# Optimization experiments

Measured on AMD Instinct MI355X. Metric: run time of the kernel, lower is better.

The kernel has to match this reference:

```python
import jax, jax.numpy as jnp
import numpy as np

NUM_HEADS = 12
NUM_PATCHES = 4096
DIM = 768
IN_DIMS = DIM // NUM_HEADS
SCALE = NUM_PATCHES ** (-0.5)
LN_EPS = 1e-5


def setup_inputs() -> dict:
    key = jax.random.key(0)
    ks = jax.random.split(key, 14)
    s = 0.02
    return {
        "x": jax.random.normal(ks[0], (16, NUM_PATCHES, DIM), dtype=jnp.float32),
        "wq": jax.random.normal(ks[1], (DIM, DIM), dtype=jnp.float32) * s,
        "bq": jnp.zeros((DIM,), dtype=jnp.float32),
        "wk": jax.random.normal(ks[2], (DIM, DIM), dtype=jnp.float32) * s,
        "bk": jnp.zeros((DIM,), dtype=jnp.float32),
        "w_g": jax.random.normal(ks[3], (NUM_PATCHES,), dtype=jnp.float32),
        "w_fc": jax.random.normal(ks[4], (IN_DIMS, DIM), dtype=jnp.float32) * s,
        "b_fc": jnp.zeros((DIM,), dtype=jnp.float32),
        "w_fc2": jax.random.normal(ks[5], (NUM_HEADS, NUM_HEADS), dtype=jnp.float32) * s,
        "b_fc2": jnp.zeros((NUM_HEADS,), dtype=jnp.float32),
        "w_proj": jax.random.normal(ks[6], (DIM, DIM), dtype=jnp.float32) * s,
        "b_proj": jnp.zeros((DIM,), dtype=jnp.float32),
        "gamma": jnp.ones((DIM,), dtype=jnp.float32),
        "beta": jnp.zeros((DIM,), dtype=jnp.float32),
    }


def layernorm(x, gamma, beta):
    mu = jnp.mean(x, axis=-1, keepdims=True)
    var = jnp.mean(jnp.square(x - mu), axis=-1, keepdims=True)
    return (x - mu) * jax.lax.rsqrt(var + LN_EPS) * gamma + beta


def reference(x, wq, bq, wk, bk, w_g, w_fc, b_fc, w_fc2, b_fc2, w_proj, b_proj, gamma, beta):
    bs, n, d = x.shape
    q = x @ wq + bq                      # (b,n,d)  fc_q
    k = x @ wk + bk                      # (b,n,d)  fc_k (reassigned x in torch)
    # query_weight = (q^T @ w_g)^T -> (b,1,d); softmax over channel dim
    qw = jnp.einsum("bnd,n->bd", q, w_g) * SCALE
    A = jax.nn.softmax(qw, axis=-1)      # (b,d)
    # G = sum_n(A * k): A is constant over n, so equals A * sum_n k
    G = A * jnp.sum(k, axis=1)           # (b,d)
    # sigmoid gating chain on pooled q
    dv = jnp.mean(q, axis=1)             # (b,d)   AdaptiveAvgPool over n
    dv = dv.reshape(bs, NUM_HEADS, IN_DIMS)
    dv = jax.nn.gelu(dv @ w_fc + b_fc, approximate=False)   # (b,H,d)
    dv = dv.reshape(bs, d, NUM_HEADS)    # reshape (not transpose), as in torch
    dv = dv @ w_fc2 + b_fc2              # (b,d,H)
    dv = jax.nn.sigmoid(jnp.mean(dv, axis=-1))               # (b,d)
    G = G * dv                           # (b,d)
    out = (G[:, None, :] * k) @ w_proj + b_proj + layernorm(k, gamma, beta)
    return out
```

## Files before the change

### kernel.cpp

```cpp
#include <hip/hip_runtime.h>
#include <hip/hip_bf16.h>
#include <math.h>

#define NB 16
#define NP 4096
#define DDIM 768
#define MTOT (NB*NP)
#define N1 1536
#define BM 128
#define BN 128
#define BK 64
#define SCALEF 0.015625f
#define LNEPS 1e-5f

typedef __attribute__((ext_vector_type(8))) short bf16x8;
typedef __attribute__((ext_vector_type(4))) float f32x4;
typedef __attribute__((ext_vector_type(4))) unsigned int u32x4;
typedef unsigned short us;

__device__ __forceinline__ us f2b(float f){
  union { float f; unsigned int u; } v; v.f = f;
  unsigned int u = v.u;
  unsigned int r = (u + 0x7FFFu + ((u >> 16) & 1u)) >> 16;
  return (us)r;
}
__device__ __forceinline__ unsigned int pack2(float a, float b){
  return (unsigned int)f2b(a) | ((unsigned int)f2b(b) << 16);
}
__device__ __forceinline__ float b2f(us h){
  union { unsigned int u; float f; } v; v.u = ((unsigned int)h) << 16;
  return v.f;
}
__device__ __forceinline__ float b2f_lo(unsigned int u){
  union { unsigned int x; float f; } v; v.x = u << 16; return v.f;
}
__device__ __forceinline__ float b2f_hi(unsigned int u){
  union { unsigned int x; float f; } v; v.x = u & 0xFFFF0000u; return v.f;
}

typedef __attribute__((address_space(1))) const unsigned int gas_u32;
typedef __attribute__((address_space(3))) unsigned int las_u32;
__device__ __forceinline__ void gl2lds16(const void* g, void* l){
  __builtin_amdgcn_global_load_lds((gas_u32*)g, (las_u32*)l, 16, 0, 0);
}

__global__ __launch_bounds__(256) void convert_x(const float* __restrict__ x,
                                                 us* __restrict__ xb){
  size_t i = ((size_t)blockIdx.x * 256 + threadIdx.x) * 8;
  const float4* s = reinterpret_cast<const float4*>(x + i);
  float4 a = s[0], b = s[1];
  u32x4 w;
  w[0] = pack2(a.x, a.y); w[1] = pack2(a.z, a.w);
  w[2] = pack2(b.x, b.y); w[3] = pack2(b.z, b.w);
  *reinterpret_cast<u32x4*>(xb + i) = w;
}

__global__ __launch_bounds__(256) void prep_w(const float* __restrict__ wq,
                                              const float* __restrict__ wk,
                                              const float* __restrict__ wp,
                                              us* __restrict__ wt1,
                                              us* __restrict__ wt2){
  int idx = blockIdx.x * 256 + threadIdx.x;
  const int tot1 = N1 * DDIM;
  if (idx < tot1){
    int n = idx / DDIM, k = idx % DDIM;
    float v = (n < DDIM) ? wq[k * DDIM + n] : wk[k * DDIM + (n - DDIM)];
    wt1[idx] = f2b(v);
  }
  int idx2 = idx - tot1;
  if (idx2 >= 0 && idx2 < DDIM * DDIM){
    int n = idx2 / DDIM, k = idx2 % DDIM;
    wt2[idx2] = f2b(wp[k * DDIM + n]);
  }
}

__global__ __launch_bounds__(256) void prep_wb(const us* __restrict__ wt2,
                                               const float* __restrict__ g,
                                               us* __restrict__ wbuf){
  size_t idx = (size_t)blockIdx.x * 256 + threadIdx.x;
  int d = (int)(idx % DDIM);
  size_t nd = idx / DDIM;
  int n = (int)(nd % DDIM);
  int b = (int)(nd / DDIM);
  float v = b2f(wt2[n * DDIM + d]) * g[(size_t)b * DDIM + d];
  wbuf[idx] = f2b(v);
}

__global__ __launch_bounds__(256) void ln_stats(const us* __restrict__ kin,
                                                float2* __restrict__ rstats){
  int row = blockIdx.x * 4 + (threadIdx.x >> 6);
  int l = threadIdx.x & 63;
  const us* rp = kin + (size_t)row * DDIM;
  float s = 0.f, q = 0.f;
  bf16x8 v = *reinterpret_cast<const bf16x8*>(rp + l * 8);
  #pragma unroll
  for (int j = 0; j < 8; ++j){ float f = b2f((us)v[j]); s += f; q += f * f; }
  uint2 w2 = *reinterpret_cast<const uint2*>(rp + 512 + l * 4);
  { float f0 = b2f_lo(w2.x), f1 = b2f_hi(w2.x), f2 = b2f_lo(w2.y), f3 = b2f_hi(w2.y);
    s += f0 + f1 + f2 + f3; q += f0*f0 + f1*f1 + f2*f2 + f3*f3; }
  #pragma unroll
  for (int off = 1; off < 64; off <<= 1){
    s += __shfl_xor(s, off);
    q += __shfl_xor(q, off);
  }
  if (l == 0){
    float mu = s * (1.0f / DDIM);
    float var = q * (1.0f / DDIM) - mu * mu;
    rstats[row] = make_float2(mu, rsqrtf(var + LNEPS));
  }
}

__global__ __launch_bounds__(256) void gemm_qk(
    const us* __restrict__ xb, const us* __restrict__ wt1,
    const float* __restrict__ bq, const float* __restrict__ bk,
    const float* __restrict__ w_g,
    us* __restrict__ kout,
    float* __restrict__ qwp, float* __restrict__ qsp, float* __restrict__ ksp)
{
  __shared__ us lds[2][2][BM * BK];

  int bid = blockIdx.x;
  int swz = (bid & 7) * ((int)gridDim.x >> 3) + (bid >> 3);
  const int NBN = N1 / BN;
  int bn = swz % NBN, bm = swz / NBN;
  int m0 = bm * BM, n0 = bn * BN;
  int t = threadIdx.x, lane = t & 63, wave = t >> 6;
  int wm = wave >> 1, wn = wave & 1;
  int lr = lane & 15, lh = lane >> 4;

  const us* pa[4]; const us* pb[4];
  #pragma unroll
  for (int i = 0; i < 4; ++i){
    int c = wave * 4 + i;
    int u = c * 64 + lane;
    int row = u >> 3, cell = u & 7;
    pa[i] = xb  + (size_t)(m0 + row) * DDIM + cell * 8;
    pb[i] = wt1 + (size_t)(n0 + row) * DDIM + cell * 8;
  }
  auto stage = [&](int bufi, int ks){
    int ko = ks * BK;
    #pragma unroll
    for (int i = 0; i < 4; ++i){
      int c = wave * 4 + i;
      gl2lds16(pa[i] + ko, &lds[bufi][0][c * 512]);
      gl2lds16(pb[i] + ko, &lds[bufi][1][c * 512]);
    }
  };

  f32x4 acc[4][4] = {};
  stage(0, 0);
  __syncthreads();
  int buf = 0;
  for (int ks = 0; ks < DDIM / BK; ++ks){
    if (ks < DDIM / BK - 1) stage(buf ^ 1, ks + 1);
    #pragma unroll
    for (int kk = 0; kk < 2; ++kk){
      bf16x8 af[4], bfr[4];
      #pragma unroll
      for (int i = 0; i < 4; ++i)
        af[i] = *reinterpret_cast<const bf16x8*>(&lds[buf][0][(wm*64 + i*16 + lr)*BK + kk*32 + lh*8]);
      #pragma unroll
      for (int i = 0; i < 4; ++i)
        bfr[i] = *reinterpret_cast<const bf16x8*>(&lds[buf][1][(wn*64 + i*16 + lr)*BK + kk*32 + lh*8]);
      #pragma unroll
      for (int i = 0; i < 4; ++i)
        #pragma unroll
        for (int j = 0; j < 4; ++j)
          acc[i][j] = __builtin_amdgcn_mfma_f32_16x16x32_bf16(af[i], bfr[j], acc[i][j], 0, 0, 0);
    }
    __syncthreads();
    buf ^= 1;
  }

  bool is_q = (n0 < DDIM);
  int b = m0 / NP, mc = (m0 % NP) / BM;
  float* part0 = reinterpret_cast<float*>(&lds[1][0][0]);
  float* part1 = part0 + BM * 8;
  us* stash = &lds[0][0][0];

  float wgv[4][4];
  if (is_q){
    #pragma unroll
    for (int mf = 0; mf < 4; ++mf)
      #pragma unroll
      for (int r = 0; r < 4; ++r)
        wgv[mf][r] = w_g[(m0 & (NP - 1)) + wm*64 + mf*16 + lh*4 + r];
  }

  float r0a[4], r1a[4];
  #pragma unroll
  for (int nf = 0; nf < 4; ++nf){
    int colb = wn*64 + nf*16 + lr;
    int col = n0 + colb;
    float bias = is_q ? bq[col] : bk[col - DDIM];
    float s0 = 0.f, s1 = 0.f;
    #pragma unroll
    for (int mf = 0; mf < 4; ++mf){
      #pragma unroll
      for (int r = 0; r < 4; ++r){
        int rowb = wm*64 + mf*16 + lh*4 + r;
        float val = acc[mf][nf][r] + bias;
        if (is_q){ s0 += wgv[mf][r] * val; s1 += val; }
        else     { s0 += val; stash[rowb * BN + colb] = f2b(val); }
      }
    }
    r0a[nf] = s0; r1a[nf] = s1;
  }
  int slot = wm * 4 + lh;
  #pragma unroll
  for (int nf = 0; nf < 4; ++nf){
    int colb = wn*64 + nf*16 + lr;
    part0[colb * 8 + slot] = r0a[nf];
    part1[colb * 8 + slot] = r1a[nf];
  }
  __syncthreads();
  if (!is_q){
    #pragma unroll
    for (int s = 0; s < 8; ++s){
      int u = s * 256 + t;
      int row = u >> 4, cu = u & 15;
      *reinterpret_cast<u32x4*>(kout + (size_t)(m0 + row) * DDIM + (n0 - DDIM) + cu * 8) =
          *reinterpret_cast<const u32x4*>(stash + row * BN + cu * 8);
    }
  }
  if (t < BM){
    float s0 = 0.f, s1 = 0.f;
    #pragma unroll
    for (int i = 0; i < 8; ++i){ s0 += part0[t * 8 + i]; s1 += part1[t * 8 + i]; }
    size_t base = ((size_t)b * 32 + mc) * DDIM;
    if (is_q){ qwp[base + n0 + t] = s0; qsp[base + n0 + t] = s1; }
    else       ksp[base + (n0 - DDIM) + t] = s0;
  }
}

__global__ __launch_bounds__(256) void combine(
    const float* __restrict__ qwp, const float* __restrict__ qsp, const float* __restrict__ ksp,
    const float* __restrict__ w_fc, const float* __restrict__ b_fc,
    const float* __restrict__ w_fc2, const float* __restrict__ b_fc2,
    float* __restrict__ g)
{
  __shared__ float smA[DDIM];
  __shared__ float smQM[DDIM];
  __shared__ float smKS[DDIM];
  __shared__ float tmat[12][DDIM];
  __shared__ float red[256];
  __shared__ float wbar[12];
  __shared__ float bbar;
  int b = blockIdx.x, t = threadIdx.x;

  for (int col = t; col < DDIM; col += 256){
    float s0 = 0.f, s1 = 0.f, s2 = 0.f;
    for (int mc = 0; mc < 32; ++mc){
      size_t base = ((size_t)b * 32 + mc) * DDIM + col;
      s0 += qwp[base]; s1 += qsp[base]; s2 += ksp[base];
    }
    smA[col] = s0 * SCALEF;
    smQM[col] = s1 * (1.0f / NP);
    smKS[col] = s2;
  }
  __syncthreads();
  float lmax = -1e30f;
  for (int col = t; col < DDIM; col += 256) lmax = fmaxf(lmax, smA[col]);
  red[t] = lmax; __syncthreads();
  for (int off = 128; off; off >>= 1){
    if (t < off) red[t] = fmaxf(red[t], red[t + off]);
    __syncthreads();
  }
  float mx = red[0];
  __syncthreads();
  float lsum = 0.f;
  for (int col = t; col < DDIM; col += 256){
    float e = __expf(smA[col] - mx);
    smA[col] = e; lsum += e;
  }
  red[t] = lsum; __syncthreads();
  for (int off = 128; off; off >>= 1){
    if (t < off) red[t] += red[t + off];
    __syncthreads();
  }
  float inv = 1.0f / red[0];
  for (int col = t; col < DDIM; col += 256) smA[col] *= inv;

  if (t < 12){
    float s = 0.f;
    for (int j = 0; j < 12; ++j) s += w_fc2[t * 12 + j];
    wbar[t] = s * (1.0f / 12.0f);
  }
  if (t == 12){
    float s = 0.f;
    for (int j = 0; j < 12; ++j) s += b_fc2[j];
    bbar = s * (1.0f / 12.0f);
  }
  __syncthreads();
  for (int idx = t; idx < 12 * DDIM; idx += 256){
    int h = idx / DDIM, j = idx % DDIM;
    float s = b_fc[j];
    const float* qm = &smQM[h * 64];
    #pragma unroll 4
    for (int i = 0; i < 64; ++i) s += qm[i] * w_fc[i * DDIM + j];
    tmat[h][j] = 0.5f * s * (1.0f + erff(s * 0.70710678118654752f));
  }
  __syncthreads();
  for (int p = t; p < DDIM; p += 256){
    float s = bbar;
    #pragma unroll
    for (int m = 0; m < 12; ++m){
      int f = p * 12 + m;
      s += tmat[f / DDIM][f % DDIM] * wbar[m];
    }
    float dv = 1.0f / (1.0f + __expf(-s));
    g[(size_t)b * DDIM + p] = smA[p] * smKS[p] * dv;
  }
}

__global__ __launch_bounds__(256) void gemm_out(
    const us* __restrict__ kin, const us* __restrict__ wbuf,
    const float2* __restrict__ rstats,
    const float* __restrict__ bp, const float* __restrict__ gamma,
    const float* __restrict__ beta,
    float* __restrict__ out)
{
  __shared__ us lds[2][2][BM * BK];

  int bid = blockIdx.x;
  int swz = (bid & 7) * ((int)gridDim.x >> 3) + (bid >> 3);
  const int NBN = DDIM / BN;
  int bn = swz % NBN, bm = swz / NBN;
  int m0 = bm * BM, n0 = bn * BN;
  int t = threadIdx.x, lane = t & 63, wave = t >> 6;
  int wm = wave >> 1, wn = wave & 1;
  int lr = lane & 15, lh = lane >> 4;
  int b = m0 / NP;
  const us* wb = wbuf + (size_t)b * DDIM * DDIM;

  const us* pa[4]; const us* pb[4];
  #pragma unroll
  for (int i = 0; i < 4; ++i){
    int c = wave * 4 + i;
    int u = c * 64 + lane;
    int row = u >> 3, cell = u & 7;
    pa[i] = kin + (size_t)(m0 + row) * DDIM + cell * 8;
    pb[i] = wb  + (size_t)(n0 + row) * DDIM + cell * 8;
  }
  auto stage = [&](int bufi, int ks){
    int ko = ks * BK;
    #pragma unroll
    for (int i = 0; i < 4; ++i){
      int c = wave * 4 + i;
      gl2lds16(pa[i] + ko, &lds[bufi][0][c * 512]);
      gl2lds16(pb[i] + ko, &lds[bufi][1][c * 512]);
    }
  };

  f32x4 acc[4][4] = {};
  stage(0, 0);
  __syncthreads();
  int buf = 0;
  for (int ks = 0; ks < DDIM / BK; ++ks){
    if (ks < DDIM / BK - 1) stage(buf ^ 1, ks + 1);
    #pragma unroll
    for (int kk = 0; kk < 2; ++kk){
      bf16x8 af[4], bfr[4];
      #pragma unroll
      for (int i = 0; i < 4; ++i)
        af[i] = *reinterpret_cast<const bf16x8*>(&lds[buf][0][(wm*64 + i*16 + lr)*BK + kk*32 + lh*8]);
      #pragma unroll
      for (int i = 0; i < 4; ++i)
        bfr[i] = *reinterpret_cast<const bf16x8*>(&lds[buf][1][(wn*64 + i*16 + lr)*BK + kk*32 + lh*8]);
      #pragma unroll
      for (int i = 0; i < 4; ++i)
        #pragma unroll
        for (int j = 0; j < 4; ++j)
          acc[i][j] = __builtin_amdgcn_mfma_f32_16x16x32_bf16(af[i], bfr[j], acc[i][j], 0, 0, 0);
    }
    __syncthreads();
    buf ^= 1;
  }

  us* stash = &lds[0][0][0];
  #pragma unroll
  for (int s = 0; s < 8; ++s){
    int u = s * 256 + t;
    int row = u >> 4, cu = u & 15;
    *reinterpret_cast<u32x4*>(stash + row * BN + cu * 8) =
        *reinterpret_cast<const u32x4*>(kin + (size_t)(m0 + row) * DDIM + n0 + cu * 8);
  }
  float muv[4][4], rsv[4][4];
  #pragma unroll
  for (int mf = 0; mf < 4; ++mf)
    #pragma unroll
    for (int r = 0; r < 4; ++r){
      float2 st = rstats[m0 + wm*64 + mf*16 + lh*4 + r];
      muv[mf][r] = st.x; rsv[mf][r] = st.y;
    }
  __syncthreads();
  #pragma unroll
  for (int nf = 0; nf < 4; ++nf){
    int colb = wn*64 + nf*16 + lr;
    int col = n0 + colb;
    float bpv = bp[col], gmv = gamma[col], btv = beta[col];
    #pragma unroll
    for (int mf = 0; mf < 4; ++mf){
      #pragma unroll
      for (int r = 0; r < 4; ++r){
        int rowb = wm*64 + mf*16 + lh*4 + r;
        float kv = b2f(stash[rowb * BN + colb]);
        acc[mf][nf][r] = acc[mf][nf][r] + bpv + (kv - muv[mf][r]) * rsv[mf][r] * gmv + btv;
      }
    }
  }
  __syncthreads();
  float* ldsf = reinterpret_cast<float*>(&lds[0][0][0]);
  #pragma unroll
  for (int nf = 0; nf < 4; ++nf){
    int colb = wn*64 + nf*16 + lr;
    #pragma unroll
    for (int mf = 0; mf < 4; ++mf)
      #pragma unroll
      for (int r = 0; r < 4; ++r)
        ldsf[(wm*64 + mf*16 + lh*4 + r) * BN + colb] = acc[mf][nf][r];
  }
  __syncthreads();
  #pragma unroll
  for (int s = 0; s < 16; ++s){
    int u = s * 256 + t;
    int row = u >> 5, cu = u & 31;
    *reinterpret_cast<float4*>(out + (size_t)(m0 + row) * DDIM + n0 + cu * 4) =
        *reinterpret_cast<const float4*>(ldsf + row * BN + cu * 4);
  }
}

extern "C" void kernel_launch(void* const* d_in, const int* in_sizes, int n_in,
                              void* d_out, int out_size, void* d_ws, size_t ws_size,
                              hipStream_t stream)
{
  const float* x      = (const float*)d_in[0];
  const float* wq     = (const float*)d_in[1];
  const float* bq     = (const float*)d_in[2];
  const float* wk     = (const float*)d_in[3];
  const float* bk     = (const float*)d_in[4];
  const float* w_g    = (const float*)d_in[5];
  const float* w_fc   = (const float*)d_in[6];
  const float* b_fc   = (const float*)d_in[7];
  const float* w_fc2  = (const float*)d_in[8];
  const float* b_fc2  = (const float*)d_in[9];
  const float* w_proj = (const float*)d_in[10];
  const float* b_proj = (const float*)d_in[11];
  const float* gamma  = (const float*)d_in[12];
  const float* beta   = (const float*)d_in[13];
  float* out = (float*)d_out;

  char* ws = (char*)d_ws;
  us*     xb    = (us*)(ws);
  us*     kbuf  = (us*)(ws + 100663296);
  us*     wt1   = (us*)(ws + 201326592);
  us*     wt2   = (us*)(ws + 203685888);
  us*     wbuf  = (us*)(ws + 204865536);
  float*  qwp   = (float*)(ws + 223739904);
  float*  qsp   = (float*)(ws + 225312768);
  float*  ksp   = (float*)(ws + 226885632);
  float*  g     = (float*)(ws + 228458496);
  float2* rstat = (float2*)(ws + 228507648);

  convert_x<<<dim3(MTOT * DDIM / (256 * 8)), dim3(256), 0, stream>>>(x, xb);
  prep_w<<<dim3((N1 * DDIM + DDIM * DDIM) / 256), dim3(256), 0, stream>>>(wq, wk, w_proj, wt1, wt2);
  gemm_qk<<<dim3((MTOT / BM) * (N1 / BN)), dim3(256), 0, stream>>>(
      xb, wt1, bq, bk, w_g, kbuf, qwp, qsp, ksp);
  ln_stats<<<dim3(MTOT / 4), dim3(256), 0, stream>>>(kbuf, rstat);
  combine<<<dim3(NB), dim3(256), 0, stream>>>(qwp, qsp, ksp, w_fc, b_fc, w_fc2, b_fc2, g);
  prep_wb<<<dim3(NB * DDIM * DDIM / 256), dim3(256), 0, stream>>>(wt2, g, wbuf);
  gemm_out<<<dim3((MTOT / BM) * (DDIM / BN)), dim3(256), 0, stream>>>(
      kbuf, wbuf, rstat, b_proj, gamma, beta, out);
}
```

Baseline: 557.1 us.

## Move both GEMMs to 256x256 tiles with quadrant-pipelined swizzled LDS and fused LN stats

Replaces the 128x128 double-buffered GEMM in both gemm_qk and gemm_out with a shared 256x256, 512-thread core. The core uses a 4-slot XOR-swizzled LDS ring, processes the tile in quadrants, interleaves loads with MFMA, and uses raw barriers, waitcnt and setprio. The gemm_qk epilogue now also emits per-row LayerNorm sum and sum-of-squares partials, so the separate ln_stats pass that re-read k is replaced by a tiny ln_reduce kernel. The larger tiles are meant to raise arithmetic intensity and cut global traffic. In exchange they use 128KB of dynamic LDS and heavy register use, which limits occupancy, and the hand-tuned waitcnt sequencing is fragile.

```diff
diff --git a/kernel.cpp b/kernel.cpp
--- a/kernel.cpp
+++ b/kernel.cpp
@@ -7,9 +7,6 @@
 #define DDIM 768
 #define MTOT (NB*NP)
 #define N1 1536
-#define BM 128
-#define BN 128
-#define BK 64
 #define SCALEF 0.015625f
 #define LNEPS 1e-5f
 
@@ -86,150 +83,206 @@
   wbuf[idx] = f2b(v);
 }
 
-__global__ __launch_bounds__(256) void ln_stats(const us* __restrict__ kin,
-                                                float2* __restrict__ rstats){
-  int row = blockIdx.x * 4 + (threadIdx.x >> 6);
-  int l = threadIdx.x & 63;
-  const us* rp = kin + (size_t)row * DDIM;
-  float s = 0.f, q = 0.f;
-  bf16x8 v = *reinterpret_cast<const bf16x8*>(rp + l * 8);
-  #pragma unroll
-  for (int j = 0; j < 8; ++j){ float f = b2f((us)v[j]); s += f; q += f * f; }
-  uint2 w2 = *reinterpret_cast<const uint2*>(rp + 512 + l * 4);
-  { float f0 = b2f_lo(w2.x), f1 = b2f_hi(w2.x), f2 = b2f_lo(w2.y), f3 = b2f_hi(w2.y);
-    s += f0 + f1 + f2 + f3; q += f0*f0 + f1*f1 + f2*f2 + f3*f3; }
-  #pragma unroll
-  for (int off = 1; off < 64; off <<= 1){
-    s += __shfl_xor(s, off);
-    q += __shfl_xor(q, off);
-  }
-  if (l == 0){
-    float mu = s * (1.0f / DDIM);
-    float var = q * (1.0f / DDIM) - mu * mu;
-    rstats[row] = make_float2(mu, rsqrtf(var + LNEPS));
-  }
-}
-
-__global__ __launch_bounds__(256) void gemm_qk(
+__global__ __launch_bounds__(256) void ln_reduce(const float* __restrict__ lnS,
+                                                 const float* __restrict__ lnQ,
+                                                 float2* __restrict__ rstats){
+  int r = blockIdx.x * 256 + threadIdx.x;
+  float s = lnS[r] + lnS[MTOT + r] + lnS[2*MTOT + r];
+  float q = lnQ[r] + lnQ[MTOT + r] + lnQ[2*MTOT + r];
+  float mu = s * (1.0f / DDIM);
+  float var = q * (1.0f / DDIM) - mu * mu;
+  rstats[r] = make_float2(mu, rsqrtf(var + LNEPS));
+}
+
+__device__ __forceinline__ void gemm256_core(const us* __restrict__ Ag,
+                                             const us* __restrict__ Bg,
+                                             us* lds, int t,
+                                             f32x4 (&acc)[4][4][2]){
+  us* ldsA = lds;
+  us* ldsB = lds + 32768;
+  const int wave = t >> 6, lane = t & 63;
+  const int wr = wave >> 2, wc = wave & 3, lr = lane & 15, lh = lane >> 4;
+  const int srow = t >> 3;
+  const int scell = (t & 7) ^ ((t >> 3) & 7);
+  const int key8 = lane & 7;
+
+  auto stage = [&](int sel, int h, int kt){
+    const us* gb = sel ? Bg : Ag;
+    us* lb = sel ? ldsB : ldsA;
+    int slot = (2*kt + h) & 3;
+    #pragma unroll
+    for (int j = 0; j < 2; ++j){
+      const us* src = gb + (size_t)(h*128 + j*64 + srow) * DDIM + kt*64 + scell*8;
+      gl2lds16(src, lb + slot*8192 + j*4096 + (wave << 9));
+    }
+  };
+
+  stage(0,0,0); stage(1,0,0); stage(1,1,0); stage(0,1,0);
+  stage(0,0,1); stage(1,0,1); stage(1,1,1); stage(0,1,1);
+  asm volatile("s_waitcnt vmcnt(8)" ::: "memory");
+  __builtin_amdgcn_s_barrier();
+
+  for (int kt = 0; kt < 12; ++kt){
+    #pragma unroll
+    for (int p = 0; p < 4; ++p){
+      const int qm = p >> 1, qn = p & 1;
+      const us* Ab = ldsA + ((2*kt + qm) & 3) * 8192;
+      const us* Bb = ldsB + ((2*kt + qn) & 3) * 8192;
+      bf16x8 av[4][2], bv[2][2];
+      #pragma unroll
+      for (int fm = 0; fm < 4; ++fm){
+        int ra = wr*64 + fm*16 + lr;
+        #pragma unroll
+        for (int kk = 0; kk < 2; ++kk)
+          av[fm][kk] = *reinterpret_cast<const bf16x8*>(
+              &Ab[ra*64 + ((((kk<<2)|lh) ^ key8) << 3)]);
+      }
+      #pragma unroll
+      for (int fn = 0; fn < 2; ++fn){
+        int rb = wc*32 + fn*16 + lr;
+        #pragma unroll
+        for (int kk = 0; kk < 2; ++kk)
+          bv[fn][kk] = *reinterpret_cast<const bf16x8*>(
+              &Bb[rb*64 + ((((kk<<2)|lh) ^ key8) << 3)]);
+      }
+      if (kt >= 1 && kt <= 10){
+        if      (p == 0) stage(0, 0, kt+1);
+        else if (p == 1) stage(1, 0, kt+1);
+        else if (p == 2) stage(1, 1, kt+1);
+        else             stage(0, 1, kt+1);
+      }
+      __builtin_amdgcn_sched_barrier(0);
+      __builtin_amdgcn_s_barrier();
+      __builtin_amdgcn_s_setprio(1);
+      #pragma unroll
+      for (int fm = 0; fm < 4; ++fm)
+        #pragma unroll
+        for (int fn = 0; fn < 2; ++fn)
+          #pragma unroll
+          for (int kk = 0; kk < 2; ++kk)
+            acc[p][fm][fn] = __builtin_amdgcn_mfma_f32_16x16x32_bf16(
+                av[fm][kk], bv[fn][kk], acc[p][fm][fn], 0, 0, 0);
+      __builtin_amdgcn_s_setprio(0);
+      if (kt < 11)      { asm volatile("s_waitcnt vmcnt(4)" ::: "memory"); }
+      else if (p == 0)  { asm volatile("s_waitcnt vmcnt(2)" ::: "memory"); }
+      else if (p == 1)  { asm volatile("s_waitcnt vmcnt(0)" ::: "memory"); }
+      __builtin_amdgcn_sched_barrier(0);
+      __builtin_amdgcn_s_barrier();
+    }
+  }
+}
+
+__global__ __launch_bounds__(512, 2) void gemm_qk(
     const us* __restrict__ xb, const us* __restrict__ wt1,
     const float* __restrict__ bq, const float* __restrict__ bk,
     const float* __restrict__ w_g,
     us* __restrict__ kout,
-    float* __restrict__ qwp, float* __restrict__ qsp, float* __restrict__ ksp)
+    float* __restrict__ qwp, float* __restrict__ qsp, float* __restrict__ ksp,
+    float* __restrict__ lnS, float* __restrict__ lnQ)
 {
-  __shared__ us lds[2][2][BM * BK];
-
+  extern __shared__ us lds[];
   int bid = blockIdx.x;
   int swz = (bid & 7) * ((int)gridDim.x >> 3) + (bid >> 3);
-  const int NBN = N1 / BN;
-  int bn = swz % NBN, bm = swz / NBN;
-  int m0 = bm * BM, n0 = bn * BN;
-  int t = threadIdx.x, lane = t & 63, wave = t >> 6;
-  int wm = wave >> 1, wn = wave & 1;
-  int lr = lane & 15, lh = lane >> 4;
-
-  const us* pa[4]; const us* pb[4];
-  #pragma unroll
-  for (int i = 0; i < 4; ++i){
-    int c = wave * 4 + i;
-    int u = c * 64 + lane;
-    int row = u >> 3, cell = u & 7;
-    pa[i] = xb  + (size_t)(m0 + row) * DDIM + cell * 8;
-    pb[i] = wt1 + (size_t)(n0 + row) * DDIM + cell * 8;
-  }
-  auto stage = [&](int bufi, int ks){
-    int ko = ks * BK;
-    #pragma unroll
-    for (int i = 0; i < 4; ++i){
-      int c = wave * 4 + i;
-      gl2lds16(pa[i] + ko, &lds[bufi][0][c * 512]);
-      gl2lds16(pb[i] + ko, &lds[bufi][1][c * 512]);
-    }
-  };
-
-  f32x4 acc[4][4] = {};
-  stage(0, 0);
-  __syncthreads();
-  int buf = 0;
-  for (int ks = 0; ks < DDIM / BK; ++ks){
-    if (ks < DDIM / BK - 1) stage(buf ^ 1, ks + 1);
-    #pragma unroll
-    for (int kk = 0; kk < 2; ++kk){
-      bf16x8 af[4], bfr[4];
-      #pragma unroll
-      for (int i = 0; i < 4; ++i)
-        af[i] = *reinterpret_cast<const bf16x8*>(&lds[buf][0][(wm*64 + i*16 + lr)*BK + kk*32 + lh*8]);
-      #pragma unroll
-      for (int i = 0; i < 4; ++i)
-        bfr[i] = *reinterpret_cast<const bf16x8*>(&lds[buf][1][(wn*64 + i*16 + lr)*BK + kk*32 + lh*8]);
-      #pragma unroll
-      for (int i = 0; i < 4; ++i)
-        #pragma unroll
-        for (int j = 0; j < 4; ++j)
-          acc[i][j] = __builtin_amdgcn_mfma_f32_16x16x32_bf16(af[i], bfr[j], acc[i][j], 0, 0, 0);
-    }
-    __syncthreads();
-    buf ^= 1;
-  }
-
+  int bn = swz % 6, bm = swz / 6;
+  int m0 = bm * 256, n0 = bn * 256;
+  int t = threadIdx.x;
+
+  f32x4 acc[4][4][2] = {};
+  gemm256_core(xb + (size_t)m0 * DDIM, wt1 + (size_t)n0 * DDIM, lds, t, acc);
+
+  int wave = t >> 6, lane = t & 63;
+  int wr = wave >> 2, wc = wave & 3, lr = lane & 15, lh = lane >> 4;
   bool is_q = (n0 < DDIM);
-  int b = m0 / NP, mc = (m0 % NP) / BM;
-  float* part0 = reinterpret_cast<float*>(&lds[1][0][0]);
-  float* part1 = part0 + BM * 8;
-  us* stash = &lds[0][0][0];
-
-  float wgv[4][4];
-  if (is_q){
-    #pragma unroll
-    for (int mf = 0; mf < 4; ++mf)
-      #pragma unroll
-      for (int r = 0; r < 4; ++r)
-        wgv[mf][r] = w_g[(m0 & (NP - 1)) + wm*64 + mf*16 + lh*4 + r];
-  }
-
-  float r0a[4], r1a[4];
-  #pragma unroll
-  for (int nf = 0; nf < 4; ++nf){
-    int colb = wn*64 + nf*16 + lr;
-    int col = n0 + colb;
-    float bias = is_q ? bq[col] : bk[col - DDIM];
-    float s0 = 0.f, s1 = 0.f;
-    #pragma unroll
-    for (int mf = 0; mf < 4; ++mf){
+  int b = m0 >> 12, mc = (m0 & (NP-1)) >> 8;
+
+  float bias[2][2];
+  #pragma unroll
+  for (int qn = 0; qn < 2; ++qn)
+    #pragma unroll
+    for (int fn = 0; fn < 2; ++fn){
+      int col = qn*128 + wc*32 + fn*16 + lr;
+      bias[qn][fn] = is_q ? bq[n0 + col] : bk[n0 - DDIM + col];
+    }
+
+  #pragma unroll
+  for (int p = 0; p < 4; ++p){
+    int qm = p >> 1, qn = p & 1;
+    #pragma unroll
+    for (int fm = 0; fm < 4; ++fm)
       #pragma unroll
       for (int r = 0; r < 4; ++r){
-        int rowb = wm*64 + mf*16 + lh*4 + r;
-        float val = acc[mf][nf][r] + bias;
-        if (is_q){ s0 += wgv[mf][r] * val; s1 += val; }
-        else     { s0 += val; stash[rowb * BN + colb] = f2b(val); }
+        int row = qm*128 + wr*64 + fm*16 + lh*4 + r;
+        #pragma unroll
+        for (int fn = 0; fn < 2; ++fn){
+          int col = qn*128 + wc*32 + fn*16 + lr;
+          lds[row*256 + (col ^ ((row & 7) << 3))] = f2b(acc[p][fm][fn][r] + bias[qn][fn]);
+        }
       }
-    }
-    r0a[nf] = s0; r1a[nf] = s1;
-  }
-  int slot = wm * 4 + lh;
-  #pragma unroll
-  for (int nf = 0; nf < 4; ++nf){
-    int colb = wn*64 + nf*16 + lr;
-    part0[colb * 8 + slot] = r0a[nf];
-    part1[colb * 8 + slot] = r1a[nf];
-  }
-  __syncthreads();
+  }
+  __syncthreads();
+
+  int c8 = t & 31, rb = t >> 5;
+  float cp[8] = {0,0,0,0,0,0,0,0};
+  float cpw[8] = {0,0,0,0,0,0,0,0};
+  float rs16[16], rq16[16];
+  #pragma unroll
+  for (int s = 0; s < 16; ++s){
+    int row = s*16 + rb;
+    u32x4 ch = *reinterpret_cast<const u32x4*>(&lds[row*256 + ((c8 ^ (row & 7)) << 3)]);
+    float v[8];
+    #pragma unroll
+    for (int i = 0; i < 4; ++i){ v[2*i] = b2f_lo(ch[i]); v[2*i+1] = b2f_hi(ch[i]); }
+    if (is_q){
+      float wg = w_g[(m0 & (NP-1)) + row];
+      #pragma unroll
+      for (int j = 0; j < 8; ++j){ cp[j] += v[j]; cpw[j] += wg * v[j]; }
+    } else {
+      *reinterpret_cast<u32x4*>(kout + (size_t)(m0+row)*DDIM + (n0 - DDIM) + c8*8) = ch;
+      float ss = 0.f, qq = 0.f;
+      #pragma unroll
+      for (int j = 0; j < 8; ++j){ cp[j] += v[j]; ss += v[j]; qq += v[j]*v[j]; }
+      rs16[s] = ss; rq16[s] = qq;
+    }
+  }
+  __syncthreads();
+  float* colP  = reinterpret_cast<float*>(lds);
+  float* colPw = colP + 4096;
+  float* rowP  = colP + 8192;
+  float* rowQ  = colP + 16384;
+  #pragma unroll
+  for (int j = 0; j < 8; ++j){
+    colP[(c8*8+j)*16 + rb] = cp[j];
+    if (is_q) colPw[(c8*8+j)*16 + rb] = cpw[j];
+  }
   if (!is_q){
     #pragma unroll
-    for (int s = 0; s < 8; ++s){
-      int u = s * 256 + t;
-      int row = u >> 4, cu = u & 15;
-      *reinterpret_cast<u32x4*>(kout + (size_t)(m0 + row) * DDIM + (n0 - DDIM) + cu * 8) =
-          *reinterpret_cast<const u32x4*>(stash + row * BN + cu * 8);
-    }
-  }
-  if (t < BM){
-    float s0 = 0.f, s1 = 0.f;
-    #pragma unroll
-    for (int i = 0; i < 8; ++i){ s0 += part0[t * 8 + i]; s1 += part1[t * 8 + i]; }
-    size_t base = ((size_t)b * 32 + mc) * DDIM;
-    if (is_q){ qwp[base + n0 + t] = s0; qsp[base + n0 + t] = s1; }
-    else       ksp[base + (n0 - DDIM) + t] = s0;
+    for (int s = 0; s < 16; ++s){
+      int row = s*16 + rb;
+      rowP[row*32 + c8] = rs16[s];
+      rowQ[row*32 + c8] = rq16[s];
+    }
+  }
+  __syncthreads();
+  if (t < 256){
+    float s0 = 0.f;
+    #pragma unroll
+    for (int i = 0; i < 16; ++i) s0 += colP[t*16 + i];
+    size_t base = ((size_t)b * 16 + mc) * DDIM;
+    if (is_q){
+      float s1 = 0.f;
+      #pragma unroll
+      for (int i = 0; i < 16; ++i) s1 += colPw[t*16 + i];
+      qwp[base + n0 + t] = s1;
+      qsp[base + n0 + t] = s0;
+    } else {
+      ksp[base + (n0 - DDIM) + t] = s0;
+      float rs_ = 0.f, rq_ = 0.f;
+      #pragma unroll
+      for (int i = 0; i < 32; ++i){ rs_ += rowP[t*32 + i]; rq_ += rowQ[t*32 + i]; }
+      int kb = bn - 3;
+      lnS[(size_t)kb * MTOT + m0 + t] = rs_;
+      lnQ[(size_t)kb * MTOT + m0 + t] = rq_;
+    }
   }
 }
 
@@ -250,8 +303,8 @@
 
   for (int col = t; col < DDIM; col += 256){
     float s0 = 0.f, s1 = 0.f, s2 = 0.f;
-    for (int mc = 0; mc < 32; ++mc){
-      size_t base = ((size_t)b * 32 + mc) * DDIM + col;
+    for (int mc = 0; mc < 16; ++mc){
+      size_t base = ((size_t)b * 16 + mc) * DDIM + col;
       s0 += qwp[base]; s1 += qsp[base]; s2 += ksp[base];
     }
     smA[col] = s0 * SCALEF;
@@ -313,120 +366,84 @@
   }
 }
 
-__global__ __launch_bounds__(256) void gemm_out(
+__global__ __launch_bounds__(512, 2) void gemm_out(
     const us* __restrict__ kin, const us* __restrict__ wbuf,
     const float2* __restrict__ rstats,
     const float* __restrict__ bp, const float* __restrict__ gamma,
     const float* __restrict__ beta,
     float* __restrict__ out)
 {
-  __shared__ us lds[2][2][BM * BK];
-
+  extern __shared__ us lds[];
   int bid = blockIdx.x;
   int swz = (bid & 7) * ((int)gridDim.x >> 3) + (bid >> 3);
-  const int NBN = DDIM / BN;
-  int bn = swz % NBN, bm = swz / NBN;
-  int m0 = bm * BM, n0 = bn * BN;
-  int t = threadIdx.x, lane = t & 63, wave = t >> 6;
-  int wm = wave >> 1, wn = wave & 1;
-  int lr = lane & 15, lh = lane >> 4;
-  int b = m0 / NP;
-  const us* wb = wbuf + (size_t)b * DDIM * DDIM;
-
-  const us* pa[4]; const us* pb[4];
-  #pragma unroll
-  for (int i = 0; i < 4; ++i){
-    int c = wave * 4 + i;
-    int u = c * 64 + lane;
-    int row = u >> 3, cell = u & 7;
-    pa[i] = kin + (size_t)(m0 + row) * DDIM + cell * 8;
-    pb[i] = wb  + (size_t)(n0 + row) * DDIM + cell * 8;
-  }
-  auto stage = [&](int bufi, int ks){
-    int ko = ks * BK;
-    #pragma unroll
-    for (int i = 0; i < 4; ++i){
-      int c = wave * 4 + i;
-      gl2lds16(pa[i] + ko, &lds[bufi][0][c * 512]);
-      gl2lds16(pb[i] + ko, &lds[bufi][1][c * 512]);
-    }
-  };
-
-  f32x4 acc[4][4] = {};
-  stage(0, 0);
-  __syncthreads();
-  int buf = 0;
-  for (int ks = 0; ks < DDIM / BK; ++ks){
-    if (ks < DDIM / BK - 1) stage(buf ^ 1, ks + 1);
-    #pragma unroll
-    for (int kk = 0; kk < 2; ++kk){
-      bf16x8 af[4], bfr[4];
-      #pragma unroll
-      for (int i = 0; i < 4; ++i)
-        af[i] = *reinterpret_cast<const bf16x8*>(&lds[buf][0][(wm*64 + i*16 + lr)*BK + kk*32 + lh*8]);
-      #pragma unroll
-      for (int i = 0; i < 4; ++i)
-        bfr[i] = *reinterpret_cast<const bf16x8*>(&lds[buf][1][(wn*64 + i*16 + lr)*BK + kk*32 + lh*8]);
-      #pragma unroll
-      for (int i = 0; i < 4; ++i)
-        #pragma unroll
-        for (int j = 0; j < 4; ++j)
-          acc[i][j] = __builtin_amdgcn_mfma_f32_16x16x32_bf16(af[i], bfr[j], acc[i][j], 0, 0, 0);
+  int bn = swz % 3, bm = swz / 3;
+  int m0 = bm * 256, n0 = bn * 256;
+  int t = threadIdx.x;
+  int b = m0 >> 12;
+
+  f32x4 acc[4][4][2] = {};
+  gemm256_core(kin + (size_t)m0 * DDIM,
+               wbuf + (size_t)b * DDIM * DDIM + (size_t)n0 * DDIM, lds, t, acc);
+
+  int wave = t >> 6, lane = t & 63;
+  int wr = wave >> 2, wc = wave & 3, lr = lane & 15, lh = lane >> 4;
+
+  #pragma unroll
+  for (int j = 0; j < 16; ++j){
+    int row = j*16 + (t >> 5);
+    const us* src = kin + (size_t)(m0 + row) * DDIM + n0 + (((t & 31) ^ (row & 7)) << 3);
+    gl2lds16(src, lds + j*4096 + (wave << 9));
+  }
+  asm volatile("s_waitcnt vmcnt(0)" ::: "memory");
+  __syncthreads();
+
+  #pragma unroll
+  for (int p = 0; p < 4; ++p){
+    int qm = p >> 1, qn = p & 1;
+    #pragma unroll
+    for (int fn = 0; fn < 2; ++fn){
+      int col = qn*128 + wc*32 + fn*16 + lr;
+      float bpv = bp[n0 + col], gmv = gamma[n0 + col], btv = beta[n0 + col];
+      #pragma unroll
+      for (int fm = 0; fm < 4; ++fm)
+        #pragma unroll
+        for (int r = 0; r < 4; ++r){
+          int row = qm*128 + wr*64 + fm*16 + lh*4 + r;
+          float2 st = rstats[m0 + row];
+          float kv = b2f(lds[row*256 + (col ^ ((row & 7) << 3))]);
+          acc[p][fm][fn][r] += bpv + (kv - st.x) * st.y * gmv + btv;
+        }
+    }
+  }
+  __syncthreads();
+
+  float* fb = reinterpret_cast<float*>(lds);
+  #pragma unroll
+  for (int h = 0; h < 2; ++h){
+    #pragma unroll
+    for (int qm2 = 0; qm2 < 2; ++qm2){
+      int p = qm2*2 + h;
+      #pragma unroll
+      for (int fm = 0; fm < 4; ++fm)
+        #pragma unroll
+        for (int r = 0; r < 4; ++r){
+          int row = qm2*128 + wr*64 + fm*16 + lh*4 + r;
+          #pragma unroll
+          for (int fn = 0; fn < 2; ++fn){
+            int c = wc*32 + fn*16 + lr;
+            fb[row*128 + (c ^ ((row & 7) << 2))] = acc[p][fm][fn][r];
+          }
+        }
     }
     __syncthreads();
-    buf ^= 1;
-  }
-
-  us* stash = &lds[0][0][0];
-  #pragma unroll
-  for (int s = 0; s < 8; ++s){
-    int u = s * 256 + t;
-    int row = u >> 4, cu = u & 15;
-    *reinterpret_cast<u32x4*>(stash + row * BN + cu * 8) =
-        *reinterpret_cast<const u32x4*>(kin + (size_t)(m0 + row) * DDIM + n0 + cu * 8);
-  }
-  float muv[4][4], rsv[4][4];
-  #pragma unroll
-  for (int mf = 0; mf < 4; ++mf)
-    #pragma unroll
-    for (int r = 0; r < 4; ++r){
-      float2 st = rstats[m0 + wm*64 + mf*16 + lh*4 + r];
-      muv[mf][r] = st.x; rsv[mf][r] = st.y;
-    }
-  __syncthreads();
-  #pragma unroll
-  for (int nf = 0; nf < 4; ++nf){
-    int colb = wn*64 + nf*16 + lr;
-    int col = n0 + colb;
-    float bpv = bp[col], gmv = gamma[col], btv = beta[col];
-    #pragma unroll
-    for (int mf = 0; mf < 4; ++mf){
-      #pragma unroll
-      for (int r = 0; r < 4; ++r){
-        int rowb = wm*64 + mf*16 + lh*4 + r;
-        float kv = b2f(stash[rowb * BN + colb]);
-        acc[mf][nf][r] = acc[mf][nf][r] + bpv + (kv - muv[mf][r]) * rsv[mf][r] * gmv + btv;
-      }
-    }
-  }
-  __syncthreads();
-  float* ldsf = reinterpret_cast<float*>(&lds[0][0][0]);
-  #pragma unroll
-  for (int nf = 0; nf < 4; ++nf){
-    int colb = wn*64 + nf*16 + lr;
-    #pragma unroll
-    for (int mf = 0; mf < 4; ++mf)
-      #pragma unroll
-      for (int r = 0; r < 4; ++r)
-        ldsf[(wm*64 + mf*16 + lh*4 + r) * BN + colb] = acc[mf][nf][r];
-  }
-  __syncthreads();
-  #pragma unroll
-  for (int s = 0; s < 16; ++s){
-    int u = s * 256 + t;
-    int row = u >> 5, cu = u & 31;
-    *reinterpret_cast<float4*>(out + (size_t)(m0 + row) * DDIM + n0 + cu * 4) =
-        *reinterpret_cast<const float4*>(ldsf + row * BN + cu * 4);
+    #pragma unroll
+    for (int s = 0; s < 16; ++s){
+      int u = s*512 + t;
+      int row = u >> 5, c4 = u & 31;
+      float4 vv = *reinterpret_cast<const float4*>(&fb[row*128 + ((c4 ^ (row & 7)) << 2)]);
+      *reinterpret_cast<float4*>(&out[(size_t)(m0 + row) * DDIM + n0 + h*128 + c4*4]) = vv;
+    }
+    __syncthreads();
   }
 }
 
@@ -457,18 +474,20 @@
   us*     wt2   = (us*)(ws + 203685888);
   us*     wbuf  = (us*)(ws + 204865536);
   float*  qwp   = (float*)(ws + 223739904);
-  float*  qsp   = (float*)(ws + 225312768);
-  float*  ksp   = (float*)(ws + 226885632);
-  float*  g     = (float*)(ws + 228458496);
-  float2* rstat = (float2*)(ws + 228507648);
+  float*  qsp   = (float*)(ws + 224526336);
+  float*  ksp   = (float*)(ws + 225312768);
+  float*  lnS   = (float*)(ws + 226099200);
+  float*  lnQ   = (float*)(ws + 226885632);
+  float*  g     = (float*)(ws + 227672064);
+  float2* rstat = (float2*)(ws + 227721216);
 
   convert_x<<<dim3(MTOT * DDIM / (256 * 8)), dim3(256), 0, stream>>>(x, xb);
   prep_w<<<dim3((N1 * DDIM + DDIM * DDIM) / 256), dim3(256), 0, stream>>>(wq, wk, w_proj, wt1, wt2);
-  gemm_qk<<<dim3((MTOT / BM) * (N1 / BN)), dim3(256), 0, stream>>>(
-      xb, wt1, bq, bk, w_g, kbuf, qwp, qsp, ksp);
-  ln_stats<<<dim3(MTOT / 4), dim3(256), 0, stream>>>(kbuf, rstat);
+  gemm_qk<<<dim3((MTOT / 256) * (N1 / 256)), dim3(512), 131072, stream>>>(
+      xb, wt1, bq, bk, w_g, kbuf, qwp, qsp, ksp, lnS, lnQ);
+  ln_reduce<<<dim3(MTOT / 256), dim3(256), 0, stream>>>(lnS, lnQ, rstat);
   combine<<<dim3(NB), dim3(256), 0, stream>>>(qwp, qsp, ksp, w_fc, b_fc, w_fc2, b_fc2, g);
   prep_wb<<<dim3(NB * DDIM * DDIM / 256), dim3(256), 0, stream>>>(wt2, g, wbuf);
-  gemm_out<<<dim3((MTOT / BM) * (DDIM / BN)), dim3(256), 0, stream>>>(
+  gemm_out<<<dim3((MTOT / 256) * (DDIM / 256)), dim3(512), 131072, stream>>>(
       kbuf, wbuf, rstat, b_proj, gamma, beta, out);
 }
```

Result: faster. 535.4 us (-3.9%).
